# Optimization experiments

Hardware: AMD Instinct MI355X
Metric: run time of the kernel (lower is better)

Reference implementation:

```python
import jax, jax.numpy as jnp
import numpy as np

B, T, C, H = 4, 2048, 1024, 16
D = C // H  # head dim = 64

def setup_inputs() -> dict:
    key = jax.random.key(0)
    k1, k2, k3 = jax.random.split(key, 3)
    y = jax.random.normal(k1, (B, T, C), dtype=jnp.float32)
    W_attn = jax.random.normal(k2, (C, 3 * C), dtype=jnp.float32) * (1.0 / np.sqrt(C))
    b_attn = jnp.zeros((3 * C,), dtype=jnp.float32)
    W_proj = jax.random.normal(k3, (C, C), dtype=jnp.float32) * (1.0 / np.sqrt(C))
    b_proj = jnp.zeros((C,), dtype=jnp.float32)
    return {"y": y, "W_attn": W_attn, "b_attn": b_attn, "W_proj": W_proj, "b_proj": b_proj}

def reference(y, W_attn, b_attn, W_proj, b_proj):
    # qkv projection: [B,T,C] @ [C,3C] -> split into q,k,v
    qkv = y @ W_attn + b_attn
    q, k, v = jnp.split(qkv, 3, axis=-1)
    # [B,T,C] -> [B,H,T,D]
    q = q.reshape(B, T, H, D).swapaxes(1, 2)
    k = k.reshape(B, T, H, D).swapaxes(1, 2)
    v = v.reshape(B, T, H, D).swapaxes(1, 2)
    # scaled dot-product attention, non-causal (config default), dropout=0
    att = jnp.einsum('bhtd,bhrd->bhtr', q, k) * (1.0 / jnp.sqrt(jnp.float32(D)))
    att = jax.nn.softmax(att, axis=-1)
    out = jnp.einsum('bhts,bhsd->bhtd', att, v)
    out = out.swapaxes(1, 2).reshape(B, T, C)
    return out @ W_proj + b_proj
```

## Files before the change

kernel.cpp:

```cpp
#include <hip/hip_runtime.h>
#include <hip/hip_bf16.h>
#include <stdint.h>

#define B_ 4
#define T_ 2048
#define C_ 1024
#define H_ 16
#define D_ 64

typedef short bf16x8 __attribute__((ext_vector_type(8)));
typedef short bf16x4 __attribute__((ext_vector_type(4)));
typedef float f32x4 __attribute__((ext_vector_type(4)));
typedef unsigned short u16;

#define HAS_M16 __has_builtin(__builtin_amdgcn_mfma_f32_16x16x16bf16_1k)

#define QSCALE 0.18033688011112042f

__device__ __forceinline__ u16 f2bf(float f) {
    __hip_bfloat16 h = __float2bfloat16(f);
    return *reinterpret_cast<u16*>(&h);
}

__device__ __forceinline__ float fexp2(float x) {
    float r;
    asm("v_exp_f32 %0, %1" : "=v"(r) : "v"(x));
    return r;
}

__device__ __forceinline__ void gload16(const void* g, void* l) {
    __builtin_amdgcn_global_load_lds(
        (const __attribute__((address_space(1))) unsigned int*)g,
        (__attribute__((address_space(3))) unsigned int*)l, 16, 0, 0);
}

__global__ void k_cast_bf16(const float* __restrict__ src, u16* __restrict__ dst, int n) {
    int i = (blockIdx.x * blockDim.x + threadIdx.x) * 4;
    if (i >= n) return;
    float4 f = *reinterpret_cast<const float4*>(src + i);
    ushort4 o;
    o.x = f2bf(f.x); o.y = f2bf(f.y); o.z = f2bf(f.z); o.w = f2bf(f.w);
    *reinterpret_cast<ushort4*>(dst + i) = o;
}

__global__ void k_transpose_bf16(const float* __restrict__ src, u16* __restrict__ dst,
                                 int R, int Cc) {
    __shared__ float tile[32][33];
    int c0 = blockIdx.x * 32, r0 = blockIdx.y * 32;
    int tx = threadIdx.x, ty = threadIdx.y;
#pragma unroll
    for (int i = 0; i < 4; i++)
        tile[ty + i * 8][tx] = src[(size_t)(r0 + ty + i * 8) * Cc + c0 + tx];
    __syncthreads();
#pragma unroll
    for (int i = 0; i < 4; i++)
        dst[(size_t)(c0 + ty + i * 8) * R + r0 + tx] = f2bf(tile[tx][ty + i * 8]);
}

template <int EPI>
__launch_bounds__(256, 2)
__global__ void k_gemm(const u16* __restrict__ A, const u16* __restrict__ Bt,
                       const float* __restrict__ bias, int K, int N,
                       float* __restrict__ outf,
                       u16* __restrict__ qw, u16* __restrict__ kw, u16* __restrict__ vw) {
    __shared__ u16 As[128 * 64];
    __shared__ u16 Bs[128 * 64];
    const int tid = threadIdx.x;
    const int lane = tid & 63, w = tid >> 6;
    const int m0 = blockIdx.x * 128, n0 = blockIdx.y * 128;
    const int wm = (w >> 1) * 64, wn = (w & 1) * 64;
    const int lr = lane & 15, lg = lane >> 4;

    f32x4 acc[4][4];
#pragma unroll
    for (int i = 0; i < 4; i++)
#pragma unroll
        for (int j = 0; j < 4; j++) acc[i][j] = (f32x4){0.f, 0.f, 0.f, 0.f};

    const int nk = K >> 6;
    for (int kt = 0; kt < nk; ++kt) {
        const int k0 = kt * 64;
#pragma unroll
        for (int i = 0; i < 4; i++) {
            int c = i * 256 + tid;
            int row = c >> 3, k8 = (c & 7) << 3;
            gload16(A + (size_t)(m0 + row) * K + k0 + k8, (char*)As + i * 4096 + w * 1024);
            gload16(Bt + (size_t)(n0 + row) * K + k0 + k8, (char*)Bs + i * 4096 + w * 1024);
        }
        __syncthreads();
#pragma unroll
        for (int kk = 0; kk < 2; ++kk) {
            bf16x8 af[4], bfr[4];
#pragma unroll
            for (int mf = 0; mf < 4; ++mf)
                af[mf] = *reinterpret_cast<const bf16x8*>(&As[(wm + mf * 16 + lr) * 64 + kk * 32 + lg * 8]);
#pragma unroll
            for (int nf = 0; nf < 4; ++nf)
                bfr[nf] = *reinterpret_cast<const bf16x8*>(&Bs[(wn + nf * 16 + lr) * 64 + kk * 32 + lg * 8]);
#pragma unroll
            for (int mf = 0; mf < 4; ++mf)
#pragma unroll
                for (int nf = 0; nf < 4; ++nf)
                    acc[mf][nf] = __builtin_amdgcn_mfma_f32_16x16x32_bf16(af[mf], bfr[nf], acc[mf][nf], 0, 0, 0);
        }
        __syncthreads();
    }

    if (EPI == 0) {
#pragma unroll
        for (int mf = 0; mf < 4; ++mf)
#pragma unroll
            for (int nf = 0; nf < 4; ++nf) {
                int ng = n0 + wn + nf * 16 + lr;
                float bs = bias[ng];
#pragma unroll
                for (int r = 0; r < 4; ++r) {
                    int mg = m0 + wm + mf * 16 + lg * 4 + r;
                    outf[(size_t)mg * N + ng] = acc[mf][nf][r] + bs;
                }
            }
    } else {
        const int sec = n0 >> 10;
        const float sc = (sec == 0) ? QSCALE : 1.0f;
#pragma unroll
        for (int mf = 0; mf < 4; ++mf)
#pragma unroll
            for (int nf = 0; nf < 4; ++nf) {
                int ng = n0 + wn + nf * 16 + lr;
                float bs = bias[ng];
                int hd = ng & 1023;
                int h = hd >> 6, d = hd & 63;
                int mgb = m0 + wm + mf * 16 + lg * 4;
                int b = mgb >> 11, t0v = mgb & 2047;
                if (sec == 2) {
                    ushort4 pk;
                    pk.x = f2bf(acc[mf][nf][0] + bs);
                    pk.y = f2bf(acc[mf][nf][1] + bs);
                    pk.z = f2bf(acc[mf][nf][2] + bs);
                    pk.w = f2bf(acc[mf][nf][3] + bs);
                    *reinterpret_cast<ushort4*>(&vw[((size_t)(b * H_ + h) * D_ + d) * T_ + t0v]) = pk;
                } else {
                    u16* dst = (sec == 0) ? qw : kw;
#pragma unroll
                    for (int r = 0; r < 4; ++r)
                        dst[((size_t)(b * H_ + h) * T_ + t0v + r) * D_ + d] = f2bf((acc[mf][nf][r] + bs) * sc);
                }
            }
    }
}

#if HAS_M16
__launch_bounds__(256, 4)
#else
__launch_bounds__(256, 3)
#endif
__global__ void k_attn(const u16* __restrict__ qw, const u16* __restrict__ kw,
                       const u16* __restrict__ vw, u16* __restrict__ attn) {
    __shared__ u16 Ks[2][64][64];
    __shared__ u16 Vs[2][64][64];
#if !HAS_M16
    __shared__ u16 pshm[4][32][64];
#endif
    const int tid = threadIdx.x, lane = tid & 63, w = tid >> 6;
    const int lr = lane & 15, lg = lane >> 4;
    const int bid = blockIdx.x;
    const int logical = (bid & 7) * 128 + (bid >> 3);
    const int bh = logical >> 4, qb = logical & 15;
    const int b = bh >> 4, h = bh & 15;
    const int q0 = qb * 128 + w * 32;
    const u16* qbase = qw + (size_t)bh * T_ * D_;
    const u16* kbase = kw + (size_t)bh * T_ * D_;
    const u16* vbase = vw + (size_t)bh * D_ * T_;

    bf16x8 qf[2][2];
#pragma unroll
    for (int jq = 0; jq < 2; jq++)
#pragma unroll
        for (int kd = 0; kd < 2; kd++)
            qf[jq][kd] = *reinterpret_cast<const bf16x8*>(
                &qbase[(size_t)(q0 + jq * 16 + lr) * D_ + kd * 32 + lg * 8]);

    auto stageK = [&](int kt, int buf) {
#pragma unroll
        for (int i = 0; i < 2; i++) {
            int idx = i * 256 + tid;
            int row = idx >> 3, ch = idx & 7;
            int gch = ch ^ (row & 7);
            gload16(kbase + ((size_t)(kt * 64 + row) * 64 + gch * 8),
                    (char*)&Ks[buf][0][0] + i * 4096 + w * 1024);
        }
    };
    auto stageV = [&](int kt, int buf) {
#pragma unroll
        for (int i = 0; i < 2; i++) {
            int idx = i * 256 + tid;
            int row = idx >> 3, ch = idx & 7;
            int gch = ch ^ (row & 7);
            gload16(vbase + ((size_t)row * T_ + kt * 64 + gch * 8),
                    (char*)&Vs[buf][0][0] + i * 4096 + w * 1024);
        }
    };

    f32x4 o[4][2];
#pragma unroll
    for (int md = 0; md < 4; md++)
#pragma unroll
        for (int jq = 0; jq < 2; jq++) o[md][jq] = (f32x4){0.f, 0.f, 0.f, 0.f};
    float l_run[2] = {0.f, 0.f};

    const int NT = T_ / 64;
    stageK(0, 0);
    stageV(0, 0);

    for (int kt = 0; kt < NT; ++kt) {
        const int cur = kt & 1;
        if (kt + 1 < NT) {
            stageK(kt + 1, cur ^ 1);
            stageV(kt + 1, cur ^ 1);
            asm volatile("s_waitcnt vmcnt(4)" ::: "memory");
        } else {
            asm volatile("s_waitcnt vmcnt(0)" ::: "memory");
        }
        __builtin_amdgcn_s_barrier();

        bf16x8 ka[4][2];
#pragma unroll
        for (int mk = 0; mk < 4; mk++)
#pragma unroll
            for (int kd = 0; kd < 2; kd++) {
                int row = mk * 16 + lr;
                int colb = (kd * 64 + lg * 16) ^ ((row & 7) << 4);
                ka[mk][kd] = *reinterpret_cast<const bf16x8*>(
                    (const char*)&Ks[cur][0][0] + row * 128 + colb);
            }

        f32x4 s[4][2];
#pragma unroll
        for (int mk = 0; mk < 4; mk++)
#pragma unroll
            for (int jq = 0; jq < 2; jq++) s[mk][jq] = (f32x4){0.f, 0.f, 0.f, 0.f};
        __builtin_amdgcn_s_setprio(1);
#pragma unroll
        for (int kd = 0; kd < 2; kd++)
#pragma unroll
            for (int mk = 0; mk < 4; mk++)
#pragma unroll
                for (int jq = 0; jq < 2; jq++)
                    s[mk][jq] = __builtin_amdgcn_mfma_f32_16x16x32_bf16(ka[mk][kd], qf[jq][kd], s[mk][jq], 0, 0, 0);
        __builtin_amdgcn_s_setprio(0);

#if HAS_M16
        bf16x4 pfrag[2][4];
#endif
#pragma unroll
        for (int jq = 0; jq < 2; jq++) {
            float psum = 0.f;
#pragma unroll
            for (int mk = 0; mk < 4; mk++) {
                float p0 = fexp2(s[mk][jq][0]);
                float p1 = fexp2(s[mk][jq][1]);
                float p2 = fexp2(s[mk][jq][2]);
                float p3 = fexp2(s[mk][jq][3]);
                psum += (p0 + p1) + (p2 + p3);
#if HAS_M16
                pfrag[jq][mk] = (bf16x4){(short)f2bf(p0), (short)f2bf(p1),
                                         (short)f2bf(p2), (short)f2bf(p3)};
#else
                ushort4 pk;
                pk.x = f2bf(p0); pk.y = f2bf(p1); pk.z = f2bf(p2); pk.w = f2bf(p3);
                int prow = jq * 16 + lr;
                int pcolb = (mk * 32 + lg * 8) ^ ((prow & 7) << 4);
                *reinterpret_cast<ushort4*>((char*)&pshm[w][0][0] + prow * 128 + pcolb) = pk;
#endif
            }
            l_run[jq] += psum;
        }

#if HAS_M16
        __builtin_amdgcn_s_setprio(1);
#pragma unroll
        for (int md = 0; md < 4; md++) {
            int row = md * 16 + lr;
#pragma unroll
            for (int mk = 0; mk < 4; mk++) {
                int colb = (mk * 32 + lg * 8) ^ ((row & 7) << 4);
                bf16x4 va = *reinterpret_cast<const bf16x4*>(
                    (const char*)&Vs[cur][0][0] + row * 128 + colb);
                o[md][0] = __builtin_amdgcn_mfma_f32_16x16x16bf16_1k(va, pfrag[0][mk], o[md][0], 0, 0, 0);
                o[md][1] = __builtin_amdgcn_mfma_f32_16x16x16bf16_1k(va, pfrag[1][mk], o[md][1], 0, 0, 0);
            }
        }
        __builtin_amdgcn_s_setprio(0);
#else
        asm volatile("s_waitcnt lgkmcnt(0)" ::: "memory");
        bf16x8 pb[2][2];
#pragma unroll
        for (int jq = 0; jq < 2; jq++)
#pragma unroll
            for (int kk = 0; kk < 2; kk++) {
                int prow = jq * 16 + lr;
                int pcolb = (kk * 64 + lg * 16) ^ ((prow & 7) << 4);
                pb[jq][kk] = *reinterpret_cast<const bf16x8*>(
                    (const char*)&pshm[w][0][0] + prow * 128 + pcolb);
            }
        bf16x8 va[4][2];
#pragma unroll
        for (int md = 0; md < 4; md++)
#pragma unroll
            for (int kk = 0; kk < 2; kk++) {
                int row = md * 16 + lr;
                int colb = (kk * 64 + lg * 16) ^ ((row & 7) << 4);
                va[md][kk] = *reinterpret_cast<const bf16x8*>(
                    (const char*)&Vs[cur][0][0] + row * 128 + colb);
            }
        __builtin_amdgcn_s_setprio(1);
#pragma unroll
        for (int md = 0; md < 4; md++)
#pragma unroll
            for (int jq = 0; jq < 2; jq++)
#pragma unroll
                for (int kk = 0; kk < 2; kk++)
                    o[md][jq] = __builtin_amdgcn_mfma_f32_16x16x32_bf16(va[md][kk], pb[jq][kk], o[md][jq], 0, 0, 0);
        __builtin_amdgcn_s_setprio(0);
#endif

        __builtin_amdgcn_s_barrier();
    }

#pragma unroll
    for (int jq = 0; jq < 2; jq++) {
        float l = l_run[jq];
        l += __shfl_xor(l, 16);
        l += __shfl_xor(l, 32);
        float rinv = 1.f / l;
        int q = q0 + jq * 16 + lr;
#pragma unroll
        for (int md = 0; md < 4; md++) {
            int d0 = md * 16 + lg * 4;
            ushort4 pk;
            pk.x = f2bf(o[md][jq][0] * rinv);
            pk.y = f2bf(o[md][jq][1] * rinv);
            pk.z = f2bf(o[md][jq][2] * rinv);
            pk.w = f2bf(o[md][jq][3] * rinv);
            *reinterpret_cast<ushort4*>(&attn[((size_t)(b * T_ + q)) * C_ + h * D_ + d0]) = pk;
        }
    }
}

extern "C" void kernel_launch(void* const* d_in, const int* in_sizes, int n_in,
                              void* d_out, int out_size, void* d_ws, size_t ws_size,
                              hipStream_t stream) {
    const float* y = (const float*)d_in[0];
    const float* W_attn = (const float*)d_in[1];
    const float* b_attn = (const float*)d_in[2];
    const float* W_proj = (const float*)d_in[3];
    const float* b_proj = (const float*)d_in[4];

    char* ws = (char*)d_ws;
    u16* y_bf = (u16*)(ws);
    u16* WaT  = (u16*)(ws + 16777216);
    u16* WpT  = (u16*)(ws + 16777216 + 6291456);
    u16* q_ws = (u16*)(ws + 25165824);
    u16* k_ws = (u16*)(ws + 25165824 + 16777216);
    u16* v_ws = (u16*)(ws + 25165824 + 33554432);
    u16* attn = (u16*)(ws + 25165824 + 50331648);

    k_cast_bf16<<<8192, 256, 0, stream>>>(y, y_bf, B_ * T_ * C_);
    k_transpose_bf16<<<dim3(96, 32), dim3(32, 8), 0, stream>>>(W_attn, WaT, 1024, 3072);
    k_transpose_bf16<<<dim3(32, 32), dim3(32, 8), 0, stream>>>(W_proj, WpT, 1024, 1024);
    k_gemm<1><<<dim3(64, 24), 256, 0, stream>>>(y_bf, WaT, b_attn, 1024, 3072,
                                                nullptr, q_ws, k_ws, v_ws);
    k_attn<<<1024, 256, 0, stream>>>(q_ws, k_ws, v_ws, attn);
    k_gemm<0><<<dim3(64, 8), 256, 0, stream>>>(attn, WpT, b_proj, 1024, 1024,
                                               (float*)d_out, nullptr, nullptr, nullptr);
}
```

Measured before the change: 214.4 us.

## Rewrite GEMM as 8-wave 128x256 tile with double-buffered swizzled LDS pipeline

Replaces the 4-wave 128x128 GEMM with an 8-wave 128x256 tile kernel. It double-buffers A and B tiles in LDS and issues the global loads for the next K-steps between MFMA groups, using explicit vmcnt waits and barriers. The LDS layout is XOR-swizzled to avoid bank conflicts, blocks are remapped so neighbouring blocks share inputs in cache, and s_setprio is raised around the MFMA groups. The aim is to hide global-load latency and raise MFMA utilisation. In exchange it uses more LDS and more barriers, hardcodes K=1024, and the epilogue mapping for the wider N tile is not shown.

Result: slower. 224.9 us (+4.9%).

```diff
diff --git a/kernel.cpp b/kernel.cpp
--- a/kernel.cpp
+++ b/kernel.cpp
@@ -58,18 +58,36 @@
 }
 
 template <int EPI>
-__launch_bounds__(256, 2)
-__global__ void k_gemm(const u16* __restrict__ A, const u16* __restrict__ Bt,
-                       const float* __restrict__ bias, int K, int N,
-                       float* __restrict__ outf,
-                       u16* __restrict__ qw, u16* __restrict__ kw, u16* __restrict__ vw) {
-    __shared__ u16 As[128 * 64];
-    __shared__ u16 Bs[128 * 64];
+__launch_bounds__(512, 2)
+__global__ void k_gemm8(const u16* __restrict__ A, const u16* __restrict__ Bt,
+                        const float* __restrict__ bias, int N,
+                        float* __restrict__ outf,
+                        u16* __restrict__ qw, u16* __restrict__ kw, u16* __restrict__ vw) {
+    constexpr int K = 1024, NK = 16, ITERS = NK / 2;
+    __shared__ u16 Asl[2][128 * 64];
+    __shared__ u16 Bsl[2][256 * 64];
     const int tid = threadIdx.x;
     const int lane = tid & 63, w = tid >> 6;
-    const int m0 = blockIdx.x * 128, n0 = blockIdx.y * 128;
-    const int wm = (w >> 1) * 64, wn = (w & 1) * 64;
     const int lr = lane & 15, lg = lane >> 4;
+    const int nwg = 64 * (N >> 8);
+    const int cpx = nwg >> 3;
+    const int swzb = (blockIdx.x & 7) * cpx + (blockIdx.x >> 3);
+    const int m0 = (swzb & 63) * 128;
+    const int n0 = (swzb >> 6) * 256;
+    const int wm = (w >> 2) * 64, wn = (w & 3) * 64;
+    const int xswz = (lr & 7) << 4;
+
+    const u16* Abase = A + (size_t)m0 * K;
+    const u16* Bbase = Bt + (size_t)n0 * K;
+
+    auto stageU = [&](u16* lunit, const u16* g) {
+#pragma unroll
+        for (int i = 0; i < 2; i++) {
+            int idx = i * 512 + tid;
+            int row = idx >> 3, ch = idx & 7, gch = ch ^ (row & 7);
+            gload16(g + (size_t)row * K + gch * 8, (char*)lunit + i * 8192 + w * 1024);
+        }
+    };
 
     f32x4 acc[4][4];
 #pragma unroll
@@ -77,33 +95,69 @@
 #pragma unroll
         for (int j = 0; j < 4; j++) acc[i][j] = (f32x4){0.f, 0.f, 0.f, 0.f};
 
-    const int nk = K >> 6;
-    for (int kt = 0; kt < nk; ++kt) {
-        const int k0 = kt * 64;
-#pragma unroll
-        for (int i = 0; i < 4; i++) {
-            int c = i * 256 + tid;
-            int row = c >> 3, k8 = (c & 7) << 3;
-            gload16(A + (size_t)(m0 + row) * K + k0 + k8, (char*)As + i * 4096 + w * 1024);
-            gload16(Bt + (size_t)(n0 + row) * K + k0 + k8, (char*)Bs + i * 4096 + w * 1024);
-        }
-        __syncthreads();
-#pragma unroll
-        for (int kk = 0; kk < 2; ++kk) {
-            bf16x8 af[4], bfr[4];
-#pragma unroll
-            for (int mf = 0; mf < 4; ++mf)
-                af[mf] = *reinterpret_cast<const bf16x8*>(&As[(wm + mf * 16 + lr) * 64 + kk * 32 + lg * 8]);
-#pragma unroll
-            for (int nf = 0; nf < 4; ++nf)
-                bfr[nf] = *reinterpret_cast<const bf16x8*>(&Bs[(wn + nf * 16 + lr) * 64 + kk * 32 + lg * 8]);
-#pragma unroll
-            for (int mf = 0; mf < 4; ++mf)
-#pragma unroll
-                for (int nf = 0; nf < 4; ++nf)
-                    acc[mf][nf] = __builtin_amdgcn_mfma_f32_16x16x32_bf16(af[mf], bfr[nf], acc[mf][nf], 0, 0, 0);
-        }
-        __syncthreads();
+    stageU(Asl[0], Abase);
+    stageU(Bsl[0], Bbase);
+    stageU(Bsl[0] + 128 * 64, Bbase + (size_t)128 * K);
+    stageU(Bsl[1], Bbase + 64);
+    stageU(Bsl[1] + 128 * 64, Bbase + (size_t)128 * K + 64);
+    asm volatile("s_waitcnt vmcnt(4)" ::: "memory");
+    __builtin_amdgcn_s_barrier();
+
+    bf16x8 bfr[4][2];
+    for (int it = 0; it < ITERS; ++it) {
+        const int t1 = 2 * it + 1;
+        const int t0n = (2 * it + 2 < NK) ? 2 * it + 2 : NK - 1;
+        const int t1n = (2 * it + 3 < NK) ? 2 * it + 3 : NK - 1;
+        const bool last = (it == ITERS - 1);
+
+#pragma unroll
+        for (int half = 0; half < 2; ++half) {
+            const char* Ab = (const char*)Asl[half];
+            const char* Bb = (const char*)Bsl[half];
+#pragma unroll
+            for (int p = 0; p < 4; ++p) {
+                bf16x8 af[2];
+                int arow = wm + p * 16 + lr;
+#pragma unroll
+                for (int kk = 0; kk < 2; kk++)
+                    af[kk] = *reinterpret_cast<const bf16x8*>(
+                        Ab + arow * 128 + ((kk * 64 + lg * 16) ^ xswz));
+                if (p == 0) {
+#pragma unroll
+                    for (int nf = 0; nf < 4; nf++) {
+                        int brow = wn + nf * 16 + lr;
+#pragma unroll
+                        for (int kk = 0; kk < 2; kk++)
+                            bfr[nf][kk] = *reinterpret_cast<const bf16x8*>(
+                                Bb + brow * 128 + ((kk * 64 + lg * 16) ^ xswz));
+                    }
+                }
+                if (half == 0) {
+                    if (p == 0)      stageU(Asl[1], Abase + t1 * 64);
+                    else if (p == 1) stageU(Bsl[0], Bbase + t0n * 64);
+                    else if (p == 2) stageU(Bsl[0] + 128 * 64, Bbase + (size_t)128 * K + t0n * 64);
+                    else {
+                        if (!last) asm volatile("s_waitcnt vmcnt(4)" ::: "memory");
+                        else       asm volatile("s_waitcnt vmcnt(0)" ::: "memory");
+                    }
+                } else {
+                    if (p == 0)      stageU(Asl[0], Abase + t0n * 64);
+                    else if (p == 1) stageU(Bsl[1], Bbase + t1n * 64);
+                    else if (p == 2) stageU(Bsl[1] + 128 * 64, Bbase + (size_t)128 * K + t1n * 64);
+                    else             asm volatile("s_waitcnt vmcnt(4)" ::: "memory");
+                }
+                __builtin_amdgcn_s_barrier();
+                __builtin_amdgcn_s_setprio(1);
+#pragma unroll
+                for (int nf = 0; nf < 4; nf++)
+#pragma unroll
+                    for (int kk = 0; kk < 2; kk++)
+                        acc[p][nf] = __builtin_amdgcn_mfma_f32_16x16x32_bf16(
+                            af[kk], bfr[nf][kk], acc[p][nf], 0, 0, 0);
+                __builtin_amdgcn_s_setprio(0);
+                __builtin_amdgcn_s_barrier();
+            }
+        }
     }
 
     if (EPI == 0) {
@@ -368,9 +422,9 @@
     k_cast_bf16<<<8192, 256, 0, stream>>>(y, y_bf, B_ * T_ * C_);
     k_transpose_bf16<<<dim3(96, 32), dim3(32, 8), 0, stream>>>(W_attn, WaT, 1024, 3072);
     k_transpose_bf16<<<dim3(32, 32), dim3(32, 8), 0, stream>>>(W_proj, WpT, 1024, 1024);
-    k_gemm<1><<<dim3(64, 24), 256, 0, stream>>>(y_bf, WaT, b_attn, 1024, 3072,
-                                                nullptr, q_ws, k_ws, v_ws);
+    k_gemm8<1><<<768, 512, 0, stream>>>(y_bf, WaT, b_attn, 3072,
+                                        nullptr, q_ws, k_ws, v_ws);
     k_attn<<<1024, 256, 0, stream>>>(q_ws, k_ws, v_ws, attn);
-    k_gemm<0><<<dim3(64, 8), 256, 0, stream>>>(attn, WpT, b_proj, 1024, 1024,
-                                               (float*)d_out, nullptr, nullptr, nullptr);
-}
+    k_gemm8<0><<<256, 512, 0, stream>>>(attn, WpT, b_proj, 1024,
+                                        (float*)d_out, nullptr, nullptr, nullptr);
+}
```

## Split attention block across 8 waves with 16 query rows each

Applied to the files above, without the earlier changes.

The attention kernel now launches 512 threads per block, with each of 8 wavefronts owning 16 query rows instead of 4 wavefronts owning 32. K/V tile staging is spread over the extra threads, so each thread issues one load per tile instead of two. The per-wave Q fragments, scores and accumulators are halved. This cuts register pressure and raises occupancy to hide latency, but each K/V fragment read from LDS is now reused for only one MFMA instead of two, which increases LDS traffic per FLOP.

New measurement: 229.1 us. 6.9% more time.

```diff
diff --git a/kernel.cpp b/kernel.cpp
--- a/kernel.cpp
+++ b/kernel.cpp
@@ -150,16 +150,16 @@
 }
 
 #if HAS_M16
-__launch_bounds__(256, 4)
+__launch_bounds__(512, 8)
 #else
-__launch_bounds__(256, 3)
+__launch_bounds__(512, 4)
 #endif
 __global__ void k_attn(const u16* __restrict__ qw, const u16* __restrict__ kw,
                        const u16* __restrict__ vw, u16* __restrict__ attn) {
     __shared__ u16 Ks[2][64][64];
     __shared__ u16 Vs[2][64][64];
 #if !HAS_M16
-    __shared__ u16 pshm[4][32][64];
+    __shared__ u16 pshm[8][16][64];
 #endif
     const int tid = threadIdx.x, lane = tid & 63, w = tid >> 6;
     const int lr = lane & 15, lg = lane >> 4;
@@ -167,46 +167,32 @@
     const int logical = (bid & 7) * 128 + (bid >> 3);
     const int bh = logical >> 4, qb = logical & 15;
     const int b = bh >> 4, h = bh & 15;
-    const int q0 = qb * 128 + w * 32;
+    const int q0 = qb * 128 + w * 16;
     const u16* qbase = qw + (size_t)bh * T_ * D_;
     const u16* kbase = kw + (size_t)bh * T_ * D_;
     const u16* vbase = vw + (size_t)bh * D_ * T_;
 
-    bf16x8 qf[2][2];
-#pragma unroll
-    for (int jq = 0; jq < 2; jq++)
-#pragma unroll
-        for (int kd = 0; kd < 2; kd++)
-            qf[jq][kd] = *reinterpret_cast<const bf16x8*>(
-                &qbase[(size_t)(q0 + jq * 16 + lr) * D_ + kd * 32 + lg * 8]);
-
+    bf16x8 qf[2];
+#pragma unroll
+    for (int kd = 0; kd < 2; kd++)
+        qf[kd] = *reinterpret_cast<const bf16x8*>(
+            &qbase[(size_t)(q0 + lr) * D_ + kd * 32 + lg * 8]);
+
+    const int srow = tid >> 3, sch = tid & 7;
+    const int sgch = sch ^ (srow & 7);
     auto stageK = [&](int kt, int buf) {
-#pragma unroll
-        for (int i = 0; i < 2; i++) {
-            int idx = i * 256 + tid;
-            int row = idx >> 3, ch = idx & 7;
-            int gch = ch ^ (row & 7);
-            gload16(kbase + ((size_t)(kt * 64 + row) * 64 + gch * 8),
-                    (char*)&Ks[buf][0][0] + i * 4096 + w * 1024);
-        }
+        gload16(kbase + ((size_t)(kt * 64 + srow) * 64 + sgch * 8),
+                (char*)&Ks[buf][0][0] + w * 1024);
     };
     auto stageV = [&](int kt, int buf) {
-#pragma unroll
-        for (int i = 0; i < 2; i++) {
-            int idx = i * 256 + tid;
-            int row = idx >> 3, ch = idx & 7;
-            int gch = ch ^ (row & 7);
-            gload16(vbase + ((size_t)row * T_ + kt * 64 + gch * 8),
-                    (char*)&Vs[buf][0][0] + i * 4096 + w * 1024);
-        }
+        gload16(vbase + ((size_t)srow * T_ + kt * 64 + sgch * 8),
+                (char*)&Vs[buf][0][0] + w * 1024);
     };
 
-    f32x4 o[4][2];
-#pragma unroll
-    for (int md = 0; md < 4; md++)
-#pragma unroll
-        for (int jq = 0; jq < 2; jq++) o[md][jq] = (f32x4){0.f, 0.f, 0.f, 0.f};
-    float l_run[2] = {0.f, 0.f};
+    f32x4 o[4];
+#pragma unroll
+    for (int md = 0; md < 4; md++) o[md] = (f32x4){0.f, 0.f, 0.f, 0.f};
+    float l_run = 0.f;
 
     const int NT = T_ / 64;
     stageK(0, 0);
@@ -217,63 +203,52 @@
         if (kt + 1 < NT) {
             stageK(kt + 1, cur ^ 1);
             stageV(kt + 1, cur ^ 1);
-            asm volatile("s_waitcnt vmcnt(4)" ::: "memory");
+            asm volatile("s_waitcnt vmcnt(2)" ::: "memory");
         } else {
             asm volatile("s_waitcnt vmcnt(0)" ::: "memory");
         }
         __builtin_amdgcn_s_barrier();
 
-        bf16x8 ka[4][2];
-#pragma unroll
-        for (int mk = 0; mk < 4; mk++)
+        f32x4 s[4];
+#pragma unroll
+        for (int mk = 0; mk < 4; mk++) s[mk] = (f32x4){0.f, 0.f, 0.f, 0.f};
+        __builtin_amdgcn_s_setprio(1);
+#pragma unroll
+        for (int mk = 0; mk < 4; mk++) {
+            int row = mk * 16 + lr;
 #pragma unroll
             for (int kd = 0; kd < 2; kd++) {
-                int row = mk * 16 + lr;
                 int colb = (kd * 64 + lg * 16) ^ ((row & 7) << 4);
-                ka[mk][kd] = *reinterpret_cast<const bf16x8*>(
+                bf16x8 ka = *reinterpret_cast<const bf16x8*>(
                     (const char*)&Ks[cur][0][0] + row * 128 + colb);
-            }
-
-        f32x4 s[4][2];
-#pragma unroll
-        for (int mk = 0; mk < 4; mk++)
-#pragma unroll
-            for (int jq = 0; jq < 2; jq++) s[mk][jq] = (f32x4){0.f, 0.f, 0.f, 0.f};
-        __builtin_amdgcn_s_setprio(1);
-#pragma unroll
-        for (int kd = 0; kd < 2; kd++)
-#pragma unroll
-            for (int mk = 0; mk < 4; mk++)
-#pragma unroll
-                for (int jq = 0; jq < 2; jq++)
-                    s[mk][jq] = __builtin_amdgcn_mfma_f32_16x16x32_bf16(ka[mk][kd], qf[jq][kd], s[mk][jq], 0, 0, 0);
+                s[mk] = __builtin_amdgcn_mfma_f32_16x16x32_bf16(ka, qf[kd], s[mk], 0, 0, 0);
+            }
+        }
         __builtin_amdgcn_s_setprio(0);
 
 #if HAS_M16
-        bf16x4 pfrag[2][4];
-#endif
-#pragma unroll
-        for (int jq = 0; jq < 2; jq++) {
+        bf16x4 pfrag[4];
+#endif
+        {
             float psum = 0.f;
 #pragma unroll
             for (int mk = 0; mk < 4; mk++) {
-                float p0 = fexp2(s[mk][jq][0]);
-                float p1 = fexp2(s[mk][jq][1]);
-                float p2 = fexp2(s[mk][jq][2]);
-                float p3 = fexp2(s[mk][jq][3]);
+                float p0 = fexp2(s[mk][0]);
+                float p1 = fexp2(s[mk][1]);
+                float p2 = fexp2(s[mk][2]);
+                float p3 = fexp2(s[mk][3]);
                 psum += (p0 + p1) + (p2 + p3);
 #if HAS_M16
-                pfrag[jq][mk] = (bf16x4){(short)f2bf(p0), (short)f2bf(p1),
-                                         (short)f2bf(p2), (short)f2bf(p3)};
+                pfrag[mk] = (bf16x4){(short)f2bf(p0), (short)f2bf(p1),
+                                     (short)f2bf(p2), (short)f2bf(p3)};
 #else
                 ushort4 pk;
                 pk.x = f2bf(p0); pk.y = f2bf(p1); pk.z = f2bf(p2); pk.w = f2bf(p3);
-                int prow = jq * 16 + lr;
-                int pcolb = (mk * 32 + lg * 8) ^ ((prow & 7) << 4);
-                *reinterpret_cast<ushort4*>((char*)&pshm[w][0][0] + prow * 128 + pcolb) = pk;
-#endif
-            }
-            l_run[jq] += psum;
+                int pcolb = (mk * 32 + lg * 8) ^ ((lr & 7) << 4);
+                *reinterpret_cast<ushort4*>((char*)&pshm[w][0][0] + lr * 128 + pcolb) = pk;
+#endif
+            }
+            l_run += psum;
         }
 
 #if HAS_M16
@@ -286,62 +261,51 @@
                 int colb = (mk * 32 + lg * 8) ^ ((row & 7) << 4);
                 bf16x4 va = *reinterpret_cast<const bf16x4*>(
                     (const char*)&Vs[cur][0][0] + row * 128 + colb);
-                o[md][0] = __builtin_amdgcn_mfma_f32_16x16x16bf16_1k(va, pfrag[0][mk], o[md][0], 0, 0, 0);
-                o[md][1] = __builtin_amdgcn_mfma_f32_16x16x16bf16_1k(va, pfrag[1][mk], o[md][1], 0, 0, 0);
+                o[md] = __builtin_amdgcn_mfma_f32_16x16x16bf16_1k(va, pfrag[mk], o[md], 0, 0, 0);
             }
         }
         __builtin_amdgcn_s_setprio(0);
 #else
         asm volatile("s_waitcnt lgkmcnt(0)" ::: "memory");
-        bf16x8 pb[2][2];
-#pragma unroll
-        for (int jq = 0; jq < 2; jq++)
+        bf16x8 pb[2];
+#pragma unroll
+        for (int kk = 0; kk < 2; kk++) {
+            int pcolb = (kk * 64 + lg * 16) ^ ((lr & 7) << 4);
+            pb[kk] = *reinterpret_cast<const bf16x8*>(
+                (const char*)&pshm[w][0][0] + lr * 128 + pcolb);
+        }
+        __builtin_amdgcn_s_setprio(1);
+#pragma unroll
+        for (int md = 0; md < 4; md++) {
+            int row = md * 16 + lr;
 #pragma unroll
             for (int kk = 0; kk < 2; kk++) {
-                int prow = jq * 16 + lr;
-                int pcolb = (kk * 64 + lg * 16) ^ ((prow & 7) << 4);
-                pb[jq][kk] = *reinterpret_cast<const bf16x8*>(
-                    (const char*)&pshm[w][0][0] + prow * 128 + pcolb);
-            }
-        bf16x8 va[4][2];
-#pragma unroll
-        for (int md = 0; md < 4; md++)
-#pragma unroll
-            for (int kk = 0; kk < 2; kk++) {
-                int row = md * 16 + lr;
                 int colb = (kk * 64 + lg * 16) ^ ((row & 7) << 4);
-                va[md][kk] = *reinterpret_cast<const bf16x8*>(
+                bf16x8 va = *reinterpret_cast<const bf16x8*>(
                     (const char*)&Vs[cur][0][0] + row * 128 + colb);
-            }
-        __builtin_amdgcn_s_setprio(1);
-#pragma unroll
-        for (int md = 0; md < 4; md++)
-#pragma unroll
-            for (int jq = 0; jq < 2; jq++)
-#pragma unroll
-                for (int kk = 0; kk < 2; kk++)
-                    o[md][jq] = __builtin_amdgcn_mfma_f32_16x16x32_bf16(va[md][kk], pb[jq][kk], o[md][jq], 0, 0, 0);
+                o[md] = __builtin_amdgcn_mfma_f32_16x16x32_bf16(va, pb[kk], o[md], 0, 0, 0);
+            }
+        }
         __builtin_amdgcn_s_setprio(0);
 #endif
 
         __builtin_amdgcn_s_barrier();
     }
 
-#pragma unroll
-    for (int jq = 0; jq < 2; jq++) {
-        float l = l_run[jq];
+    {
+        float l = l_run;
         l += __shfl_xor(l, 16);
         l += __shfl_xor(l, 32);
         float rinv = 1.f / l;
-        int q = q0 + jq * 16 + lr;
+        int q = q0 + lr;
 #pragma unroll
         for (int md = 0; md < 4; md++) {
             int d0 = md * 16 + lg * 4;
             ushort4 pk;
-            pk.x = f2bf(o[md][jq][0] * rinv);
-            pk.y = f2bf(o[md][jq][1] * rinv);
-            pk.z = f2bf(o[md][jq][2] * rinv);
-            pk.w = f2bf(o[md][jq][3] * rinv);
+            pk.x = f2bf(o[md][0] * rinv);
+            pk.y = f2bf(o[md][1] * rinv);
+            pk.z = f2bf(o[md][2] * rinv);
+            pk.w = f2bf(o[md][3] * rinv);
             *reinterpret_cast<ushort4*>(&attn[((size_t)(b * T_ + q)) * C_ + h * D_ + d0]) = pk;
         }
     }
@@ -370,7 +334,7 @@
     k_transpose_bf16<<<dim3(32, 32), dim3(32, 8), 0, stream>>>(W_proj, WpT, 1024, 1024);
     k_gemm<1><<<dim3(64, 24), 256, 0, stream>>>(y_bf, WaT, b_attn, 1024, 3072,
                                                 nullptr, q_ws, k_ws, v_ws);
-    k_attn<<<1024, 256, 0, stream>>>(q_ws, k_ws, v_ws, attn);
+    k_attn<<<1024, 512, 0, stream>>>(q_ws, k_ws, v_ws, attn);
     k_gemm<0><<<dim3(64, 8), 256, 0, stream>>>(attn, WpT, b_proj, 1024, 1024,
                                                (float*)d_out, nullptr, nullptr, nullptr);
 }
```

## Permute K rows so softmax probabilities feed 16x16x32 MFMA directly from registers

Applied to the files above, without the earlier changes.

Reorders which K rows each lane loads for the QK^T MFMA, with a matching LDS swizzle, so each lane's eight exp'd scores form a contiguous 32-wide bf16 fragment for the PV MFMA. The PV product then uses the 16x16x32 instruction, halving the MFMA count relative to the 16x16x16 path. The QK and softmax work is also split into two 32-key groups to lower register pressure. The non-M16 LDS fallback path is removed, and correctness depends on the key permutation matching the V layout exactly.

Result: faster. 200.1 us (-6.7%).

```diff
diff --git a/kernel.cpp b/kernel.cpp
--- a/kernel.cpp
+++ b/kernel.cpp
@@ -9,11 +9,8 @@
 #define D_ 64
 
 typedef short bf16x8 __attribute__((ext_vector_type(8)));
-typedef short bf16x4 __attribute__((ext_vector_type(4)));
 typedef float f32x4 __attribute__((ext_vector_type(4)));
 typedef unsigned short u16;
-
-#define HAS_M16 __has_builtin(__builtin_amdgcn_mfma_f32_16x16x16bf16_1k)
 
 #define QSCALE 0.18033688011112042f
 
@@ -149,18 +146,11 @@
     }
 }
 
-#if HAS_M16
 __launch_bounds__(256, 4)
-#else
-__launch_bounds__(256, 3)
-#endif
 __global__ void k_attn(const u16* __restrict__ qw, const u16* __restrict__ kw,
                        const u16* __restrict__ vw, u16* __restrict__ attn) {
     __shared__ u16 Ks[2][64][64];
     __shared__ u16 Vs[2][64][64];
-#if !HAS_M16
-    __shared__ u16 pshm[4][32][64];
-#endif
     const int tid = threadIdx.x, lane = tid & 63, w = tid >> 6;
     const int lr = lane & 15, lg = lane >> 4;
     const int bid = blockIdx.x;
@@ -185,7 +175,7 @@
         for (int i = 0; i < 2; i++) {
             int idx = i * 256 + tid;
             int row = idx >> 3, ch = idx & 7;
-            int gch = ch ^ (row & 7);
+            int gch = ch ^ ((row & 3) | (((row >> 3) & 1) << 2));
             gload16(kbase + ((size_t)(kt * 64 + row) * 64 + gch * 8),
                     (char*)&Ks[buf][0][0] + i * 4096 + w * 1024);
         }
@@ -207,6 +197,9 @@
 #pragma unroll
         for (int jq = 0; jq < 2; jq++) o[md][jq] = (f32x4){0.f, 0.f, 0.f, 0.f};
     float l_run[2] = {0.f, 0.f};
+
+    const int karow_base = ((lr >> 2) << 3) + (lr & 3);
+    const int skl = ((lr & 3) | (((lr >> 2) & 1) << 2)) << 4;
 
     const int NT = T_ / 64;
     stageK(0, 0);
@@ -223,106 +216,59 @@
         }
         __builtin_amdgcn_s_barrier();
 
-        bf16x8 ka[4][2];
-#pragma unroll
-        for (int mk = 0; mk < 4; mk++)
-#pragma unroll
-            for (int kd = 0; kd < 2; kd++) {
-                int row = mk * 16 + lr;
-                int colb = (kd * 64 + lg * 16) ^ ((row & 7) << 4);
-                ka[mk][kd] = *reinterpret_cast<const bf16x8*>(
-                    (const char*)&Ks[cur][0][0] + row * 128 + colb);
-            }
-
-        f32x4 s[4][2];
-#pragma unroll
-        for (int mk = 0; mk < 4; mk++)
-#pragma unroll
-            for (int jq = 0; jq < 2; jq++) s[mk][jq] = (f32x4){0.f, 0.f, 0.f, 0.f};
-        __builtin_amdgcn_s_setprio(1);
-#pragma unroll
-        for (int kd = 0; kd < 2; kd++)
-#pragma unroll
-            for (int mk = 0; mk < 4; mk++)
+        bf16x8 pfrag[2][2];
+#pragma unroll
+        for (int g = 0; g < 2; g++) {
+            f32x4 st[2][2];
+#pragma unroll
+            for (int t = 0; t < 2; t++)
+#pragma unroll
+                for (int jq = 0; jq < 2; jq++) st[t][jq] = (f32x4){0.f, 0.f, 0.f, 0.f};
+            __builtin_amdgcn_s_setprio(1);
+#pragma unroll
+            for (int t = 0; t < 2; t++) {
+                int row = g * 32 + karow_base + t * 4;
+#pragma unroll
+                for (int kd = 0; kd < 2; kd++) {
+                    bf16x8 ka = *reinterpret_cast<const bf16x8*>(
+                        (const char*)&Ks[cur][0][0] + row * 128 + ((kd * 64 + lg * 16) ^ skl));
+#pragma unroll
+                    for (int jq = 0; jq < 2; jq++)
+                        st[t][jq] = __builtin_amdgcn_mfma_f32_16x16x32_bf16(ka, qf[jq][kd], st[t][jq], 0, 0, 0);
+                }
+            }
+            __builtin_amdgcn_s_setprio(0);
+#pragma unroll
+            for (int jq = 0; jq < 2; jq++) {
+                float p0 = fexp2(st[0][jq][0]), p1 = fexp2(st[0][jq][1]);
+                float p2 = fexp2(st[0][jq][2]), p3 = fexp2(st[0][jq][3]);
+                float p4 = fexp2(st[1][jq][0]), p5 = fexp2(st[1][jq][1]);
+                float p6 = fexp2(st[1][jq][2]), p7 = fexp2(st[1][jq][3]);
+                l_run[jq] += ((p0 + p1) + (p2 + p3)) + ((p4 + p5) + (p6 + p7));
+                pfrag[jq][g] = (bf16x8){(short)f2bf(p0), (short)f2bf(p1),
+                                        (short)f2bf(p2), (short)f2bf(p3),
+                                        (short)f2bf(p4), (short)f2bf(p5),
+                                        (short)f2bf(p6), (short)f2bf(p7)};
+            }
+        }
+
+#pragma unroll
+        for (int g = 0; g < 2; g++) {
+            bf16x8 va[4];
+#pragma unroll
+            for (int md = 0; md < 4; md++) {
+                int row = md * 16 + lr;
+                va[md] = *reinterpret_cast<const bf16x8*>(
+                    (const char*)&Vs[cur][0][0] + row * 128 + ((g * 64 + lg * 16) ^ ((row & 7) << 4)));
+            }
+            __builtin_amdgcn_s_setprio(1);
+#pragma unroll
+            for (int md = 0; md < 4; md++)
 #pragma unroll
                 for (int jq = 0; jq < 2; jq++)
-                    s[mk][jq] = __builtin_amdgcn_mfma_f32_16x16x32_bf16(ka[mk][kd], qf[jq][kd], s[mk][jq], 0, 0, 0);
-        __builtin_amdgcn_s_setprio(0);
-
-#if HAS_M16
-        bf16x4 pfrag[2][4];
-#endif
-#pragma unroll
-        for (int jq = 0; jq < 2; jq++) {
-            float psum = 0.f;
-#pragma unroll
-            for (int mk = 0; mk < 4; mk++) {
-                float p0 = fexp2(s[mk][jq][0]);
-                float p1 = fexp2(s[mk][jq][1]);
-                float p2 = fexp2(s[mk][jq][2]);
-                float p3 = fexp2(s[mk][jq][3]);
-                psum += (p0 + p1) + (p2 + p3);
-#if HAS_M16
-                pfrag[jq][mk] = (bf16x4){(short)f2bf(p0), (short)f2bf(p1),
-                                         (short)f2bf(p2), (short)f2bf(p3)};
-#else
-                ushort4 pk;
-                pk.x = f2bf(p0); pk.y = f2bf(p1); pk.z = f2bf(p2); pk.w = f2bf(p3);
-                int prow = jq * 16 + lr;
-                int pcolb = (mk * 32 + lg * 8) ^ ((prow & 7) << 4);
-                *reinterpret_cast<ushort4*>((char*)&pshm[w][0][0] + prow * 128 + pcolb) = pk;
-#endif
-            }
-            l_run[jq] += psum;
-        }
-
-#if HAS_M16
-        __builtin_amdgcn_s_setprio(1);
-#pragma unroll
-        for (int md = 0; md < 4; md++) {
-            int row = md * 16 + lr;
-#pragma unroll
-            for (int mk = 0; mk < 4; mk++) {
-                int colb = (mk * 32 + lg * 8) ^ ((row & 7) << 4);
-                bf16x4 va = *reinterpret_cast<const bf16x4*>(
-                    (const char*)&Vs[cur][0][0] + row * 128 + colb);
-                o[md][0] = __builtin_amdgcn_mfma_f32_16x16x16bf16_1k(va, pfrag[0][mk], o[md][0], 0, 0, 0);
-                o[md][1] = __builtin_amdgcn_mfma_f32_16x16x16bf16_1k(va, pfrag[1][mk], o[md][1], 0, 0, 0);
-            }
-        }
-        __builtin_amdgcn_s_setprio(0);
-#else
-        asm volatile("s_waitcnt lgkmcnt(0)" ::: "memory");
-        bf16x8 pb[2][2];
-#pragma unroll
-        for (int jq = 0; jq < 2; jq++)
-#pragma unroll
-            for (int kk = 0; kk < 2; kk++) {
-                int prow = jq * 16 + lr;
-                int pcolb = (kk * 64 + lg * 16) ^ ((prow & 7) << 4);
-                pb[jq][kk] = *reinterpret_cast<const bf16x8*>(
-                    (const char*)&pshm[w][0][0] + prow * 128 + pcolb);
-            }
-        bf16x8 va[4][2];
-#pragma unroll
-        for (int md = 0; md < 4; md++)
-#pragma unroll
-            for (int kk = 0; kk < 2; kk++) {
-                int row = md * 16 + lr;
-                int colb = (kk * 64 + lg * 16) ^ ((row & 7) << 4);
-                va[md][kk] = *reinterpret_cast<const bf16x8*>(
-                    (const char*)&Vs[cur][0][0] + row * 128 + colb);
-            }
-        __builtin_amdgcn_s_setprio(1);
-#pragma unroll
-        for (int md = 0; md < 4; md++)
-#pragma unroll
-            for (int jq = 0; jq < 2; jq++)
-#pragma unroll
-                for (int kk = 0; kk < 2; kk++)
-                    o[md][jq] = __builtin_amdgcn_mfma_f32_16x16x32_bf16(va[md][kk], pb[jq][kk], o[md][jq], 0, 0, 0);
-        __builtin_amdgcn_s_setprio(0);
-#endif
+                    o[md][jq] = __builtin_amdgcn_mfma_f32_16x16x32_bf16(va[md], pfrag[jq][g], o[md][jq], 0, 0, 0);
+            __builtin_amdgcn_s_setprio(0);
+        }
 
         __builtin_amdgcn_s_barrier();
     }
```
